# Kernel optimization log

Measured on AMD Instinct MI355X. Metric: run time of the kernel, lower is better.

The kernel has to match this reference:

```python
import jax, jax.numpy as jnp
import numpy as np

N = 100000      # nodes
E = 1600000     # directed edges (before self-loops)
IN = 128        # in_channels
H = 4           # heads
C = 32          # out_channels per head
SLOPE = 0.2     # PyG GATConv default negative_slope


def setup_inputs() -> dict:
    key = jax.random.key(0)
    k_x, k_e, k_w, k_as, k_ad = jax.random.split(key, 5)
    x = jax.random.normal(k_x, (N, IN), dtype=jnp.float32)
    edge_index = jax.random.randint(k_e, (2, E), 0, N, dtype=jnp.int32)
    # learned params of GATConv(IN, C, heads=H, concat=False)
    W = jax.random.normal(k_w, (IN, H * C), dtype=jnp.float32) / np.sqrt(IN)
    att_src = jax.random.normal(k_as, (H, C), dtype=jnp.float32) * 0.1
    att_dst = jax.random.normal(k_ad, (H, C), dtype=jnp.float32) * 0.1
    bias = jnp.zeros((C,), dtype=jnp.float32)
    return {"x": x, "edge_index": edge_index, "W": W,
            "att_src": att_src, "att_dst": att_dst, "bias": bias}


def reference(x, edge_index, W, att_src, att_dst, bias):
    # PyG GATConv default add_self_loops=True
    loops = jnp.arange(N, dtype=edge_index.dtype)
    src = jnp.concatenate([edge_index[0], loops])  # message sources j
    dst = jnp.concatenate([edge_index[1], loops])  # message targets i

    # linear projection per head: [N, H, C]
    xp = (x @ W).reshape(N, H, C)

    # per-node attention logits: [N, H]
    a_src = jnp.einsum('nhc,hc->nh', xp, att_src)
    a_dst = jnp.einsum('nhc,hc->nh', xp, att_dst)

    # per-edge logits + leaky relu: [E', H]
    e = jax.nn.leaky_relu(a_src[src] + a_dst[dst], SLOPE)

    # segment softmax over incoming edges of each destination node
    e_max = jax.ops.segment_max(e, dst, num_segments=N)          # [N, H]
    e_exp = jnp.exp(e - e_max[dst])                              # [E', H]
    denom = jax.ops.segment_sum(e_exp, dst, num_segments=N)      # [N, H]
    alpha = e_exp / denom[dst]                                   # [E', H]
    # (attention dropout p=0.6 is inactive in eval mode)

    # weighted scatter-add aggregation: [N, H, C]
    msg = alpha[:, :, None] * xp[src]
    out = jax.ops.segment_sum(msg, dst, num_segments=N)

    # concat=False -> mean over heads, then bias; GATLayer applies relu
    out = out.mean(axis=1) + bias
    return jax.nn.relu(out)
```

## Files before the change

### kernel.cpp

```cpp
#include <hip/hip_runtime.h>
#include <cstdint>
#include <cstddef>

#define NNODE 100000
#define NEDGE 1600000
#define INC   128
#define HC    128
#define NH    4
#define CPH   32
#define NPART 8
#define NP8   (NNODE * NPART)
#define SLOPE 0.2f

#define LRELU(v) fmaxf((v), SLOPE*(v))

typedef _Float16 half4 __attribute__((ext_vector_type(4)));

static inline size_t align256(size_t x){ return (x + 255) & ~(size_t)255; }

__global__ __launch_bounds__(256) void proj_kernel(
    const float* __restrict__ x, const float* __restrict__ W,
    const float* __restrict__ att_src, const float* __restrict__ att_dst,
    _Float16* __restrict__ xp16, float* __restrict__ a_src,
    float* __restrict__ a_dst)
{
    __shared__ float xs[32 * 128];
    const int tid = threadIdx.x;
    const int cg  = tid & 31;
    const int rg  = tid >> 5;
    const int row0 = blockIdx.x * 32;

    {
        const float4* xg = (const float4*)(x + (size_t)row0 * INC);
        float4* xs4 = (float4*)xs;
        #pragma unroll
        for (int i = 0; i < 4; ++i) xs4[tid + 256 * i] = xg[tid + 256 * i];
    }
    __syncthreads();

    float4 a0 = {0,0,0,0}, a1 = {0,0,0,0}, a2 = {0,0,0,0}, a3 = {0,0,0,0};
    const float* xr = xs + rg * 4 * 128;

    #pragma unroll 8
    for (int k = 0; k < 128; ++k) {
        const float4 w = *(const float4*)(W + k * HC + cg * 4);
        const float x0 = xr[k];
        const float x1 = xr[128 + k];
        const float x2 = xr[256 + k];
        const float x3 = xr[384 + k];
        a0.x = fmaf(w.x, x0, a0.x); a0.y = fmaf(w.y, x0, a0.y);
        a0.z = fmaf(w.z, x0, a0.z); a0.w = fmaf(w.w, x0, a0.w);
        a1.x = fmaf(w.x, x1, a1.x); a1.y = fmaf(w.y, x1, a1.y);
        a1.z = fmaf(w.z, x1, a1.z); a1.w = fmaf(w.w, x1, a1.w);
        a2.x = fmaf(w.x, x2, a2.x); a2.y = fmaf(w.y, x2, a2.y);
        a2.z = fmaf(w.z, x2, a2.z); a2.w = fmaf(w.w, x2, a2.w);
        a3.x = fmaf(w.x, x3, a3.x); a3.y = fmaf(w.y, x3, a3.y);
        a3.z = fmaf(w.z, x3, a3.z); a3.w = fmaf(w.w, x3, a3.w);
    }

    {
        half4* d0 = (half4*)(xp16 + (size_t)(row0 + rg * 4) * HC);
        half4* d1 = (half4*)(xp16 + (size_t)(row0 + rg * 4 + 1) * HC);
        half4* d2 = (half4*)(xp16 + (size_t)(row0 + rg * 4 + 2) * HC);
        half4* d3 = (half4*)(xp16 + (size_t)(row0 + rg * 4 + 3) * HC);
        d0[cg] = half4{(_Float16)a0.x, (_Float16)a0.y, (_Float16)a0.z, (_Float16)a0.w};
        d1[cg] = half4{(_Float16)a1.x, (_Float16)a1.y, (_Float16)a1.z, (_Float16)a1.w};
        d2[cg] = half4{(_Float16)a2.x, (_Float16)a2.y, (_Float16)a2.z, (_Float16)a2.w};
        d3[cg] = half4{(_Float16)a3.x, (_Float16)a3.y, (_Float16)a3.z, (_Float16)a3.w};
    }

    const float4 ats = ((const float4*)att_src)[cg];
    const float4 atd = ((const float4*)att_dst)[cg];
    const int h = cg >> 3;
    #pragma unroll
    for (int i = 0; i < 4; ++i) {
        const float4 a = (i == 0) ? a0 : (i == 1) ? a1 : (i == 2) ? a2 : a3;
        float s = a.x*ats.x + a.y*ats.y + a.z*ats.z + a.w*ats.w;
        float d = a.x*atd.x + a.y*atd.y + a.z*atd.z + a.w*atd.w;
        s += __shfl_xor(s, 1); s += __shfl_xor(s, 2); s += __shfl_xor(s, 4);
        d += __shfl_xor(d, 1); d += __shfl_xor(d, 2); d += __shfl_xor(d, 4);
        if ((cg & 7) == 0) {
            const int row = row0 + rg * 4 + i;
            a_src[(size_t)row * NH + h] = s;
            a_dst[(size_t)row * NH + h] = d;
        }
    }
}

__global__ void count_seq_kernel(const int* __restrict__ ei,
                                 int* __restrict__ deg,
                                 int* __restrict__ seq)
{
    const int t4 = (blockIdx.x * 256 + threadIdx.x) * 4;
    const int p = blockIdx.x & (NPART - 1);
    if (t4 < NEDGE) {
        const int4 d4 = *(const int4*)(ei + NEDGE + t4);
        int4 s4;
        s4.x = atomicAdd(&deg[p * NNODE + d4.x], 1);
        s4.y = atomicAdd(&deg[p * NNODE + d4.y], 1);
        s4.z = atomicAdd(&deg[p * NNODE + d4.z], 1);
        s4.w = atomicAdd(&deg[p * NNODE + d4.w], 1);
        *(int4*)(seq + t4) = s4;
    }
}

__global__ __launch_bounds__(256) void scan_sums_kernel(
    const int* __restrict__ deg, int* __restrict__ bsums)
{
    __shared__ int lds[4];
    const int tid = threadIdx.x, lane = tid & 63, wid = tid >> 6;
    const int base = blockIdx.x * 4096 + tid * 16;
    int s = 0;
    #pragma unroll
    for (int i = 0; i < 16; ++i) {
        const int idx = base + i;
        if (idx < NP8) s += deg[idx];
    }
    #pragma unroll
    for (int off = 32; off; off >>= 1) s += __shfl_xor(s, off);
    if (lane == 0) lds[wid] = s;
    __syncthreads();
    if (tid == 0) bsums[blockIdx.x] = lds[0] + lds[1] + lds[2] + lds[3];
}

__global__ __launch_bounds__(256) void scan_partials_kernel(
    int* __restrict__ bsums, int nb)
{
    __shared__ int lds[4];
    const int tid = threadIdx.x, lane = tid & 63, wid = tid >> 6;
    const int v = (tid < nb) ? bsums[tid] : 0;
    int incl = v;
    #pragma unroll
    for (int off = 1; off < 64; off <<= 1) {
        const int u = __shfl_up(incl, off);
        if (lane >= off) incl += u;
    }
    if (lane == 63) lds[wid] = incl;
    __syncthreads();
    int wb = 0;
    for (int w = 0; w < wid; ++w) wb += lds[w];
    if (tid < nb) bsums[tid] = wb + incl - v;
}

__global__ __launch_bounds__(256) void scan_final_kernel(
    const int* __restrict__ deg, const int* __restrict__ bsums,
    int* __restrict__ offs)
{
    __shared__ int lds[4];
    const int tid = threadIdx.x, lane = tid & 63, wid = tid >> 6;
    const int base = blockIdx.x * 4096 + tid * 16;
    int v[16]; int s = 0;
    #pragma unroll
    for (int i = 0; i < 16; ++i) {
        const int idx = base + i;
        v[i] = (idx < NP8) ? deg[idx] : 0;
        s += v[i];
    }
    int incl = s;
    #pragma unroll
    for (int off = 1; off < 64; off <<= 1) {
        const int u = __shfl_up(incl, off);
        if (lane >= off) incl += u;
    }
    if (lane == 63) lds[wid] = incl;
    __syncthreads();
    int wb = 0;
    for (int w = 0; w < wid; ++w) wb += lds[w];
    int excl = bsums[blockIdx.x] + wb + incl - s;
    #pragma unroll
    for (int i = 0; i < 16; ++i) {
        const int idx = base + i;
        if (idx < NP8) offs[idx] = excl;
        excl += v[i];
    }
    if (blockIdx.x == 0 && tid == 0) offs[NP8] = NEDGE;
}

__global__ void scatter_kernel(const int* __restrict__ ei,
                               const int* __restrict__ offs,
                               const int* __restrict__ seq,
                               int* __restrict__ csr)
{
    const int t4 = (blockIdx.x * 256 + threadIdx.x) * 4;
    const int p = blockIdx.x & (NPART - 1);
    if (t4 < NEDGE) {
        const int4 d4 = *(const int4*)(ei + NEDGE + t4);
        const int4 s4 = *(const int4*)(ei + t4);
        const int4 q4 = *(const int4*)(seq + t4);
        csr[offs[p * NNODE + d4.x] + q4.x] = s4.x;
        csr[offs[p * NNODE + d4.y] + q4.y] = s4.y;
        csr[offs[p * NNODE + d4.z] + q4.z] = s4.z;
        csr[offs[p * NNODE + d4.w] + q4.w] = s4.w;
    }
}

__global__ __launch_bounds__(256) void aggregate_kernel(
    const _Float16* __restrict__ xp16, const float* __restrict__ a_src,
    const float* __restrict__ a_dst, const int* __restrict__ offs,
    const int* __restrict__ csr, const float* __restrict__ bias,
    float* __restrict__ out)
{
    __shared__ float p_lds[4][2][32][4];
    __shared__ int   j_lds[4][2][32];

    const int lane = threadIdx.x & 63;
    const int wid  = threadIdx.x >> 6;
    const int half = lane >> 5;
    const int sl   = lane & 31;
    const int node = blockIdx.x * 8 + wid * 2 + half;
    const int h    = sl >> 3;

    int s_val = 0, len = 0;
    if (sl < 8) {
        const int o0 = offs[sl * NNODE + node];
        const int o1 = offs[sl * NNODE + node + 1];
        s_val = o0; len = o1 - o0;
    }
    int incl = len;
    #pragma unroll
    for (int o = 1; o < 8; o <<= 1) {
        const int u = __shfl_up(incl, o, 32);
        if (sl >= o) incl += u;
    }
    const int excl = incl - len;
    int s_arr[8], b_arr[8];
    #pragma unroll
    for (int q = 0; q < 8; ++q) {
        s_arr[q] = __shfl(s_val, q, 32);
        b_arr[q] = __shfl(excl,  q, 32);
    }
    const int D = __shfl(incl, 7, 32);

    const float4 ad = ((const float4*)a_dst)[node];
    const float4 as = ((const float4*)a_src)[node];

    const float lself = (h == 0) ? LRELU(as.x + ad.x)
                      : (h == 1) ? LRELU(as.y + ad.y)
                      : (h == 2) ? LRELU(as.z + ad.z)
                                 : LRELU(as.w + ad.w);
    const float pself = __expf(lself);
    float den = pself;
    float4 acc;
    {
        const half4 hv = *(const half4*)(xp16 + (size_t)node * HC + 4 * sl);
        acc.x = pself * (float)hv.x; acc.y = pself * (float)hv.y;
        acc.z = pself * (float)hv.z; acc.w = pself * (float)hv.w;
    }

    float* pme = &p_lds[wid][half][sl][0];
    int*   jme = &j_lds[wid][half][sl];
    const float* pw = &p_lds[wid][half][0][h];
    const int*   jw = &j_lds[wid][half][0];

    for (int base = 0; base < D; base += 32) {
        const int cnt = min(32, D - base);
        if (sl < cnt) {
            const int v = base + sl;
            int sp = s_arr[0], ex = b_arr[0];
            #pragma unroll
            for (int q = 1; q < 8; ++q) {
                const bool c = (v >= b_arr[q]);
                sp = c ? s_arr[q] : sp;
                ex = c ? b_arr[q] : ex;
            }
            const int j = csr[sp + v - ex];
            const float4 aj = ((const float4*)a_src)[j];
            const float p0 = __expf(LRELU(aj.x + ad.x));
            const float p1 = __expf(LRELU(aj.y + ad.y));
            const float p2 = __expf(LRELU(aj.z + ad.z));
            const float p3 = __expf(LRELU(aj.w + ad.w));
            *(float4*)pme = make_float4(p0, p1, p2, p3);
            *jme = j;
        }

        asm volatile("s_waitcnt lgkmcnt(0)" ::: "memory");

        int t = 0;
        for (; t + 3 < cnt; t += 4) {
            const int j0 = jw[t], j1 = jw[t+1], j2 = jw[t+2], j3 = jw[t+3];
            const float q0 = pw[4*t], q1 = pw[4*t+4], q2 = pw[4*t+8], q3 = pw[4*t+12];
            const half4 v0 = *(const half4*)(xp16 + (size_t)j0 * HC + 4 * sl);
            const half4 v1 = *(const half4*)(xp16 + (size_t)j1 * HC + 4 * sl);
            const half4 v2 = *(const half4*)(xp16 + (size_t)j2 * HC + 4 * sl);
            const half4 v3 = *(const half4*)(xp16 + (size_t)j3 * HC + 4 * sl);
            den += q0 + q1 + q2 + q3;
            acc.x = fmaf(q0, (float)v0.x, acc.x); acc.y = fmaf(q0, (float)v0.y, acc.y);
            acc.z = fmaf(q0, (float)v0.z, acc.z); acc.w = fmaf(q0, (float)v0.w, acc.w);
            acc.x = fmaf(q1, (float)v1.x, acc.x); acc.y = fmaf(q1, (float)v1.y, acc.y);
            acc.z = fmaf(q1, (float)v1.z, acc.z); acc.w = fmaf(q1, (float)v1.w, acc.w);
            acc.x = fmaf(q2, (float)v2.x, acc.x); acc.y = fmaf(q2, (float)v2.y, acc.y);
            acc.z = fmaf(q2, (float)v2.z, acc.z); acc.w = fmaf(q2, (float)v2.w, acc.w);
            acc.x = fmaf(q3, (float)v3.x, acc.x); acc.y = fmaf(q3, (float)v3.y, acc.y);
            acc.z = fmaf(q3, (float)v3.z, acc.z); acc.w = fmaf(q3, (float)v3.w, acc.w);
        }
        for (; t < cnt; ++t) {
            const int   jt = jw[t];
            const float pt = pw[4*t];
            const half4 hv = *(const half4*)(xp16 + (size_t)jt * HC + 4 * sl);
            den += pt;
            acc.x = fmaf(pt, (float)hv.x, acc.x); acc.y = fmaf(pt, (float)hv.y, acc.y);
            acc.z = fmaf(pt, (float)hv.z, acc.z); acc.w = fmaf(pt, (float)hv.w, acc.w);
        }
    }

    const float inv = 1.0f / den;
    float4 r;
    r.x = acc.x * inv; r.y = acc.y * inv; r.z = acc.z * inv; r.w = acc.w * inv;
    r.x += __shfl_xor(r.x, 8); r.x += __shfl_xor(r.x, 16);
    r.y += __shfl_xor(r.y, 8); r.y += __shfl_xor(r.y, 16);
    r.z += __shfl_xor(r.z, 8); r.z += __shfl_xor(r.z, 16);
    r.w += __shfl_xor(r.w, 8); r.w += __shfl_xor(r.w, 16);
    if (sl < 8) {
        const float4 b = ((const float4*)bias)[sl];
        float4 o;
        o.x = fmaxf(0.25f * r.x + b.x, 0.f);
        o.y = fmaxf(0.25f * r.y + b.y, 0.f);
        o.z = fmaxf(0.25f * r.z + b.z, 0.f);
        o.w = fmaxf(0.25f * r.w + b.w, 0.f);
        *(float4*)(out + (size_t)node * CPH + 4 * sl) = o;
    }
}

extern "C" void kernel_launch(void* const* d_in, const int* in_sizes, int n_in,
                              void* d_out, int out_size, void* d_ws, size_t ws_size,
                              hipStream_t stream)
{
    const float* x       = (const float*)d_in[0];
    const int*   ei      = (const int*)d_in[1];
    const float* W       = (const float*)d_in[2];
    const float* att_src = (const float*)d_in[3];
    const float* att_dst = (const float*)d_in[4];
    const float* bias    = (const float*)d_in[5];
    float*       out     = (float*)d_out;

    char* ws = (char*)d_ws;
    size_t off = 0;
    auto alloc = [&](size_t bytes) -> void* {
        void* p = ws + off;
        off = align256(off + bytes);
        return p;
    };
    _Float16* xp16 = (_Float16*)alloc((size_t)NNODE * HC * sizeof(_Float16));
    float* a_src  = (float*)alloc((size_t)NNODE * NH * sizeof(float));
    float* a_dst  = (float*)alloc((size_t)NNODE * NH * sizeof(float));
    int*   deg    = (int*)alloc((size_t)NP8 * sizeof(int));
    int*   seq    = (int*)alloc((size_t)NEDGE * sizeof(int));
    int*   offs   = (int*)alloc((size_t)(NP8 + 1) * sizeof(int));
    int*   csr    = (int*)alloc((size_t)NEDGE * sizeof(int));
    int*   bsums  = (int*)alloc(1024);

    hipMemsetAsync(deg, 0, (size_t)NP8 * sizeof(int), stream);

    proj_kernel<<<NNODE / 32, 256, 0, stream>>>(x, W, att_src, att_dst, xp16, a_src, a_dst);

    constexpr int EB = (NEDGE / 4 + 255) / 256;
    count_seq_kernel<<<EB, 256, 0, stream>>>(ei, deg, seq);

    constexpr int NB = (NP8 + 4095) / 4096;
    scan_sums_kernel<<<NB, 256, 0, stream>>>(deg, bsums);
    scan_partials_kernel<<<1, 256, 0, stream>>>(bsums, NB);
    scan_final_kernel<<<NB, 256, 0, stream>>>(deg, bsums, offs);

    scatter_kernel<<<EB, 256, 0, stream>>>(ei, offs, seq, csr);
    aggregate_kernel<<<NNODE / 8, 256, 0, stream>>>(xp16, a_src, a_dst, offs, csr, bias, out);
}
```

Measured before the change: 321.7 us.

## Use fp16 MFMA for the node projection and split logits into a separate kernel

```diff
diff --git a/kernel.cpp b/kernel.cpp
--- a/kernel.cpp
+++ b/kernel.cpp
@@ -11,79 +11,118 @@
 #define NPART 8
 #define NP8   (NNODE * NPART)
 #define SLOPE 0.2f
+#define KP    136
 
 #define LRELU(v) fmaxf((v), SLOPE*(v))
 
 typedef _Float16 half4 __attribute__((ext_vector_type(4)));
+typedef _Float16 half2v __attribute__((ext_vector_type(2)));
+typedef _Float16 f16x8 __attribute__((ext_vector_type(8)));
+typedef float    f32x4 __attribute__((ext_vector_type(4)));
 
 static inline size_t align256(size_t x){ return (x + 255) & ~(size_t)255; }
 
+__global__ void wprep_kernel(const float* __restrict__ W, _Float16* __restrict__ wt16)
+{
+    const int idx = blockIdx.x * 256 + threadIdx.x;
+    const int k = idx >> 7, c = idx & 127;
+    wt16[c * 128 + k] = (_Float16)W[k * 128 + c];
+}
+
 __global__ __launch_bounds__(256) void proj_kernel(
-    const float* __restrict__ x, const float* __restrict__ W,
-    const float* __restrict__ att_src, const float* __restrict__ att_dst,
-    _Float16* __restrict__ xp16, float* __restrict__ a_src,
+    const float* __restrict__ x, const _Float16* __restrict__ wt16,
+    _Float16* __restrict__ xp16)
+{
+    __shared__ _Float16 wt_s[128 * KP];
+    __shared__ _Float16 x_s[64 * KP];
+
+    const int tid  = threadIdx.x;
+    const int lane = tid & 63;
+    const int w    = tid >> 6;
+    const int row0 = blockIdx.x * 64;
+
+    #pragma unroll
+    for (int i = 0; i < 16; ++i) {
+        const int idx = i * 256 + tid;
+        const int r = idx >> 5, c4 = idx & 31;
+        *(half4*)(wt_s + r * KP + c4 * 4) = *(const half4*)(wt16 + r * 128 + c4 * 4);
+    }
+    #pragma unroll
+    for (int i = 0; i < 8; ++i) {
+        const int idx = i * 256 + tid;
+        const int r = idx >> 5, c4 = idx & 31;
+        const int row = row0 + r;
+        half4 hv;
+        if (row < NNODE) {
+            const float4 v = *(const float4*)(x + (size_t)row * INC + c4 * 4);
+            hv = half4{(_Float16)v.x, (_Float16)v.y, (_Float16)v.z, (_Float16)v.w};
+        } else {
+            hv = half4{(_Float16)0.f, (_Float16)0.f, (_Float16)0.f, (_Float16)0.f};
+        }
+        *(half4*)(x_s + r * KP + c4 * 4) = hv;
+    }
+    __syncthreads();
+
+    const int l15 = lane & 15;
+    const int q   = lane >> 4;
+
+    f32x4 acc[8];
+    #pragma unroll
+    for (int n = 0; n < 8; ++n) acc[n] = f32x4{0.f, 0.f, 0.f, 0.f};
+
+    #pragma unroll
+    for (int kc = 0; kc < 4; ++kc) {
+        const f16x8 a = *(const f16x8*)(x_s + (16 * w + l15) * KP + kc * 32 + q * 8);
+        #pragma unroll
+        for (int n = 0; n < 8; ++n) {
+            const f16x8 b = *(const f16x8*)(wt_s + (16 * n + l15) * KP + kc * 32 + q * 8);
+            acc[n] = __builtin_amdgcn_mfma_f32_16x16x32_f16(a, b, acc[n], 0, 0, 0);
+        }
+    }
+
+    __syncthreads();
+    #pragma unroll
+    for (int n = 0; n < 8; ++n)
+        #pragma unroll
+        for (int r = 0; r < 4; ++r)
+            x_s[(16 * w + q * 4 + r) * KP + 16 * n + l15] = (_Float16)acc[n][r];
+    __syncthreads();
+
+    #pragma unroll
+    for (int i = 0; i < 8; ++i) {
+        const int idx = i * 256 + tid;
+        const int r = idx >> 5, c4 = idx & 31;
+        const int row = row0 + r;
+        if (row < NNODE)
+            *(half4*)(xp16 + (size_t)row * HC + c4 * 4) = *(const half4*)(x_s + r * KP + c4 * 4);
+    }
+}
+
+__global__ __launch_bounds__(256) void logits_kernel(
+    const _Float16* __restrict__ xp16, const float* __restrict__ att_src,
+    const float* __restrict__ att_dst, float* __restrict__ a_src,
     float* __restrict__ a_dst)
 {
-    __shared__ float xs[32 * 128];
-    const int tid = threadIdx.x;
-    const int cg  = tid & 31;
-    const int rg  = tid >> 5;
-    const int row0 = blockIdx.x * 32;
-
-    {
-        const float4* xg = (const float4*)(x + (size_t)row0 * INC);
-        float4* xs4 = (float4*)xs;
-        #pragma unroll
-        for (int i = 0; i < 4; ++i) xs4[tid + 256 * i] = xg[tid + 256 * i];
-    }
-    __syncthreads();
-
-    float4 a0 = {0,0,0,0}, a1 = {0,0,0,0}, a2 = {0,0,0,0}, a3 = {0,0,0,0};
-    const float* xr = xs + rg * 4 * 128;
-
-    #pragma unroll 8
-    for (int k = 0; k < 128; ++k) {
-        const float4 w = *(const float4*)(W + k * HC + cg * 4);
-        const float x0 = xr[k];
-        const float x1 = xr[128 + k];
-        const float x2 = xr[256 + k];
-        const float x3 = xr[384 + k];
-        a0.x = fmaf(w.x, x0, a0.x); a0.y = fmaf(w.y, x0, a0.y);
-        a0.z = fmaf(w.z, x0, a0.z); a0.w = fmaf(w.w, x0, a0.w);
-        a1.x = fmaf(w.x, x1, a1.x); a1.y = fmaf(w.y, x1, a1.y);
-        a1.z = fmaf(w.z, x1, a1.z); a1.w = fmaf(w.w, x1, a1.w);
-        a2.x = fmaf(w.x, x2, a2.x); a2.y = fmaf(w.y, x2, a2.y);
-        a2.z = fmaf(w.z, x2, a2.z); a2.w = fmaf(w.w, x2, a2.w);
-        a3.x = fmaf(w.x, x3, a3.x); a3.y = fmaf(w.y, x3, a3.y);
-        a3.z = fmaf(w.z, x3, a3.z); a3.w = fmaf(w.w, x3, a3.w);
-    }
-
-    {
-        half4* d0 = (half4*)(xp16 + (size_t)(row0 + rg * 4) * HC);
-        half4* d1 = (half4*)(xp16 + (size_t)(row0 + rg * 4 + 1) * HC);
-        half4* d2 = (half4*)(xp16 + (size_t)(row0 + rg * 4 + 2) * HC);
-        half4* d3 = (half4*)(xp16 + (size_t)(row0 + rg * 4 + 3) * HC);
-        d0[cg] = half4{(_Float16)a0.x, (_Float16)a0.y, (_Float16)a0.z, (_Float16)a0.w};
-        d1[cg] = half4{(_Float16)a1.x, (_Float16)a1.y, (_Float16)a1.z, (_Float16)a1.w};
-        d2[cg] = half4{(_Float16)a2.x, (_Float16)a2.y, (_Float16)a2.z, (_Float16)a2.w};
-        d3[cg] = half4{(_Float16)a3.x, (_Float16)a3.y, (_Float16)a3.z, (_Float16)a3.w};
-    }
-
-    const float4 ats = ((const float4*)att_src)[cg];
-    const float4 atd = ((const float4*)att_dst)[cg];
-    const int h = cg >> 3;
-    #pragma unroll
-    for (int i = 0; i < 4; ++i) {
-        const float4 a = (i == 0) ? a0 : (i == 1) ? a1 : (i == 2) ? a2 : a3;
-        float s = a.x*ats.x + a.y*ats.y + a.z*ats.z + a.w*ats.w;
-        float d = a.x*atd.x + a.y*atd.y + a.z*atd.z + a.w*atd.w;
-        s += __shfl_xor(s, 1); s += __shfl_xor(s, 2); s += __shfl_xor(s, 4);
-        d += __shfl_xor(d, 1); d += __shfl_xor(d, 2); d += __shfl_xor(d, 4);
-        if ((cg & 7) == 0) {
-            const int row = row0 + rg * 4 + i;
-            a_src[(size_t)row * NH + h] = s;
-            a_dst[(size_t)row * NH + h] = d;
-        }
+    const int lane = threadIdx.x & 63;
+    const int wid  = threadIdx.x >> 6;
+    const int node = blockIdx.x * 4 + wid;
+    if (node >= NNODE) return;
+
+    const half2v xh = *(const half2v*)(xp16 + (size_t)node * HC + 2 * lane);
+    const float x0 = (float)xh[0], x1 = (float)xh[1];
+    const float2 as = ((const float2*)att_src)[lane];
+    const float2 ad = ((const float2*)att_dst)[lane];
+    float s = x0 * as.x + x1 * as.y;
+    float d = x0 * ad.x + x1 * ad.y;
+    #pragma unroll
+    for (int off = 8; off; off >>= 1) {
+        s += __shfl_xor(s, off);
+        d += __shfl_xor(d, off);
+    }
+    if ((lane & 15) == 0) {
+        const int h = lane >> 4;
+        a_src[(size_t)node * NH + h] = s;
+        a_dst[(size_t)node * NH + h] = d;
     }
 }
 
@@ -341,6 +380,7 @@
         return p;
     };
     _Float16* xp16 = (_Float16*)alloc((size_t)NNODE * HC * sizeof(_Float16));
+    _Float16* wt16 = (_Float16*)alloc((size_t)HC * INC * sizeof(_Float16));
     float* a_src  = (float*)alloc((size_t)NNODE * NH * sizeof(float));
     float* a_dst  = (float*)alloc((size_t)NNODE * NH * sizeof(float));
     int*   deg    = (int*)alloc((size_t)NP8 * sizeof(int));
@@ -351,7 +391,9 @@
 
     hipMemsetAsync(deg, 0, (size_t)NP8 * sizeof(int), stream);
 
-    proj_kernel<<<NNODE / 32, 256, 0, stream>>>(x, W, att_src, att_dst, xp16, a_src, a_dst);
+    wprep_kernel<<<64, 256, 0, stream>>>(W, wt16);
+    proj_kernel<<<(NNODE + 63) / 64, 256, 0, stream>>>(x, wt16, xp16);
+    logits_kernel<<<(NNODE + 3) / 4, 256, 0, stream>>>(xp16, att_src, att_dst, a_src, a_dst);
 
     constexpr int EB = (NEDGE / 4 + 255) / 256;
     count_seq_kernel<<<EB, 256, 0, stream>>>(ei, deg, seq);
```

Result: faster. 295.4 us (-8.2%).
